# Optimization experiments

Measured on AMD Instinct MI355X. Metric: run time of the kernel, lower is better.

Reference implementation:

```python
import jax, jax.numpy as jnp
import numpy as np

N = 50000        # num_nodes
E = 800000       # num edges (avg degree 16)
IN = 512         # embedding_dim[0]
H = 128          # hidden_dim = embedding_dim[1]
C = 64           # out_dim = n_classes = embedding_dim[-1]
L = 3            # layer_num = len(embedding_dim) - 1


def _lin(k, fan_in, fan_out):
    s = 1.0 / np.sqrt(fan_in)
    k1, k2 = jax.random.split(k)
    W = jax.random.uniform(k1, (fan_in, fan_out), jnp.float32, -s, s)
    b = jax.random.uniform(k2, (fan_out,), jnp.float32, -s, s)
    return W, b


def setup_inputs() -> dict:
    key = jax.random.key(0)
    ks = jax.random.split(key, 12)
    d = {}
    d["x"] = jax.random.normal(ks[0], (N, IN), jnp.float32)
    d["edge_index"] = jax.random.randint(ks[1], (2, E), 0, N)
    # pseudo_mlp: in_dim -> 512 -> 64 -> out_dim
    d["Wp1"], d["bp1"] = _lin(ks[2], IN, 512)
    d["Wp2"], d["bp2"] = _lin(ks[3], 512, 64)
    d["Wp3"], d["bp3"] = _lin(ks[4], 64, C)
    # parsing_mats[0] (only ln=0 is used in learn_soft_edge3), init ones/scaling_factor
    d["parsing0"] = jnp.ones((C, C), jnp.float32) / 2.0 + 0.01 * jax.random.normal(ks[5], (C, C), jnp.float32)
    # GCNConv weights (PyG style: linear without bias, bias added after aggregation)
    d["Wg0"], d["bg0"] = _lin(ks[6], IN, H)
    d["Wg1"], d["bg1"] = _lin(ks[7], H, H)
    d["Wg2"], d["bg2"] = _lin(ks[8], H, H)
    # JK 'cat' -> lin1 input is (layer_num-1)*hidden
    d["Wl1"], d["bl1"] = _lin(ks[9], (L - 1) * H, H)
    d["Wl2"], d["bl2"] = _lin(ks[10], H, C)
    return d


def gcn_conv(x, W, b, edge_index, ew, n):
    """PyG GCNConv with per-edge weight ew, add_self_loops=True (loop weight 1)."""
    xw = x @ W                                           # [N, F_out]
    row, col = edge_index[0], edge_index[1]
    loop = jnp.arange(n)
    row2 = jnp.concatenate([row, loop])
    col2 = jnp.concatenate([col, loop])
    ew2 = jnp.concatenate([ew, jnp.ones((n,), xw.dtype)])
    deg = jax.ops.segment_sum(ew2, col2, num_segments=n)
    dis = jnp.where(deg > 0, jax.lax.rsqrt(deg), 0.0)    # deg^-1/2, inf -> 0
    norm = dis[row2] * ew2 * dis[col2]                   # [E+N]
    out = jax.ops.segment_sum(norm[:, None] * xw[row2], col2, num_segments=n)
    return out + b


def soft_edge_weight(x, edge_index, Wp1, bp1, Wp2, bp2, Wp3, bp3, parsing0):
    """learn_soft_edge3: bilinear form start^T * relu(2*P) * end per edge.
    Original materializes an [E,C,C] outer product then bmm + diagonal; the
    diagonal-sum equals einsum('ek,ed,dk->e', start, end, parsing), computed
    here as a fused small matmul + elementwise reduce (same math)."""
    h = jax.nn.relu(x @ Wp1 + bp1)
    h = jax.nn.relu(h @ Wp2 + bp2)
    logits = h @ Wp3 + bp3                               # [N, C]
    parsing = jax.nn.relu(2.0 * parsing0)                # scaling_factor = 2
    s = logits[edge_index[0]]                            # [E, C] start
    e = logits[edge_index[1]]                            # [E, C] end
    ew = jnp.sum((e @ parsing) * s, axis=-1)             # [E]
    mean = ew.mean()
    var = jnp.var(ew, ddof=1)                            # torch .var() is unbiased
    return (ew - mean) * jnp.sqrt(1e-4 / var) + 1.0


def reference(x, edge_index, Wp1, bp1, Wp2, bp2, Wp3, bp3, parsing0,
              Wg0, bg0, Wg1, bg1, Wg2, bg2, Wl1, bl1, Wl2, bl2):
    n = x.shape[0]
    ew = soft_edge_weight(x, edge_index, Wp1, bp1, Wp2, bp2, Wp3, bp3, parsing0)
    # layer 0
    x1 = jax.nn.relu(gcn_conv(x, Wg0, bg0, edge_index, ew, n))
    xs = [x1]
    # ln = 1 (not last): conv -> relu -> (dropout off in eval) -> append
    x2 = jax.nn.relu(gcn_conv(x1, Wg1, bg1, edge_index, ew, n))
    xs.append(x2)
    # ln = 2 (last layer): computed in original but loop breaks before append;
    # jump(xs) overwrites x, so the last conv's output never reaches the output.
    xj = jnp.concatenate(xs, axis=-1)                    # JK 'cat' -> [N, (L-1)*H]
    out = jax.nn.relu(xj @ Wl1 + bl1)
    out = out @ Wl2 + bl2                                # [N, C]
    return out
```

## Files before the change

### kernel.cpp

```cpp
#include <hip/hip_runtime.h>
#include <hip/hip_bf16.h>
#include <cmath>
#include <cstring>

#define NNODES 50000
#define NEDGES 800000
#define IND    512
#define HD     128
#define CD     64

typedef __bf16 bf16x8 __attribute__((ext_vector_type(8)));
typedef float  f32x4  __attribute__((ext_vector_type(4)));
typedef const __attribute__((address_space(1))) unsigned int* gu32p;
typedef __attribute__((address_space(3))) unsigned int* lu32p;

static const size_t XJ_B   = 0;
static const size_t HID_B  = 25600000;
static const size_t H1_B   = 51200000;
static const size_t XW_B   = 102400000;
static const size_t H2_B   = 115200000;
static const size_t LG_B   = 121600000;
static const size_t PE_B   = 128000000;
static const size_t WT_B   = 134400000;
static const size_t CSRR_B = 135300000;
static const size_t EWC_B  = 138500000;
static const size_t CSRW_B = 141700000;
static const size_t CNT_B  = 144900000;
static const size_t S_B    = 145100000;
static const size_t ZERO_BYTES = 200016;
static const size_t RP_B   = 145100016;
static const size_t WOFF_B = 145300020;
static const size_t INCL_B = 145500020;
static const size_t BSUM_B = 145700020;
static const size_t ST_B   = 145701044;
static const size_t DIS_B  = 145701052;

static const size_t WP1T_O = 0;
static const size_t WG0T_O = 524288;
static const size_t WP2T_O = 655360;
static const size_t WP3T_O = 720896;
static const size_t W2T_O  = 729088;
static const size_t WG1T_O = 737280;
static const size_t WL1T_O = 770048;
static const size_t WL2T_O = 835584;
static const size_t BG1_O  = 851968;
static const size_t BG3_O  = 854528;

struct WD { const float* s; __hip_bfloat16* d; int K; int N; };
struct WP { WD w[7]; };

__global__ __launch_bounds__(256) void transpose_cast_all(WP p)
{
    WD d = p.w[blockIdx.y];
    int i = blockIdx.x * 256 + threadIdx.x;
    if (i >= d.K * d.N) return;
    int k = i % d.K, n = i / d.K;
    d.d[i] = __float2bfloat16(d.s[(size_t)k * d.N + n]);
}

__global__ __launch_bounds__(256) void combine_p0(
    const float* __restrict__ Wp3, const float* __restrict__ bp3,
    const float* __restrict__ P0, const float* __restrict__ bp1,
    __hip_bfloat16* __restrict__ W2t, float* __restrict__ bias_g1,
    float* __restrict__ bias_g3)
{
    int b = blockIdx.x;
    if (b < 16) {
        int i = b * 256 + threadIdx.x;
        int k = i >> 6, n = i & 63;
        float s = 0.f;
        for (int j = 0; j < 64; j++)
            s += Wp3[k * 64 + j] * fmaxf(2.f * P0[j * 64 + n], 0.f);
        W2t[n * 64 + k] = __float2bfloat16(s);
    } else if (b == 16) {
        int n = threadIdx.x;
        if (n < 64) {
            float s = 0.f;
            for (int j = 0; j < 64; j++)
                s += bp3[j] * fmaxf(2.f * P0[j * 64 + n], 0.f);
            bias_g3[n] = bp3[n];
            bias_g3[64 + n] = s;
        }
    } else {
        int i = (b - 17) * 256 + threadIdx.x;
        if (i < 512) bias_g1[i] = bp1[i];
        else if (i < 640) bias_g1[i] = 0.f;
    }
}

template<int BN, int WN, int CAST_A>
__global__ __launch_bounds__(256) void gemm_mfma(
    const void* __restrict__ Ap, int lda,
    const __hip_bfloat16* __restrict__ Bt, int ldb,
    const float* __restrict__ bias,
    void* __restrict__ Cout, int ldc,
    void* __restrict__ Cout2, int ldc2, int splitN,
    int M, int K, int do_relu, int out_bf16)
{
    constexpr int BF = WN / 16;
    constexpr int BPASS = BN / 64;
    constexpr int AST = CAST_A ? 40 : 32;
    __shared__ __bf16 As[128 * AST];
    __shared__ __bf16 Bs[BN * 32];

    const int NC = gridDim.x, NR = gridDim.y;
    int g = blockIdx.y * NC + blockIdx.x;
    int per = NC * 8;
    int nfull = (NR >> 3) * per;
    int rowt, colt;
    if (g < nfull) {
        int grp = g / per, rem = g % per;
        rowt = grp * 8 + (rem & 7);
        colt = rem >> 3;
    } else {
        int rem = g - nfull;
        int tail = NR - (NR >> 3) * 8;
        rowt = (NR >> 3) * 8 + rem % tail;
        colt = rem / tail;
    }

    const int t = threadIdx.x;
    const int row0 = rowt * 128;
    const int col0 = colt * BN;

    const int wv   = t >> 6;
    const int lane = t & 63;
    const int quad = lane >> 4;
    const int l16  = lane & 15;
    const int wrow = (wv >> 1) * 64;
    const int wcol = (wv & 1) * WN;

    const int subrow = lane >> 2;
    const int kchunk = (lane & 3) ^ (subrow & 3);
    const int subkg  = kchunk * 8;

    f32x4 acc[4][BF] = {};

    for (int k0 = 0; k0 < K; k0 += 32) {
        if (CAST_A) {
            const float* Af = (const float*)Ap;
            #pragma unroll
            for (int p = 0; p < 4; p++) {
                int idx = t + p * 256;
                int r = idx >> 3, kg = (idx & 7) * 4;
                int m = row0 + r;
                if (m > M - 1) m = M - 1;
                float4 v = *(const float4*)(Af + (size_t)m * lda + k0 + kg);
                __hip_bfloat16 o[4] __attribute__((aligned(8)));
                o[0] = __float2bfloat16(v.x); o[1] = __float2bfloat16(v.y);
                o[2] = __float2bfloat16(v.z); o[3] = __float2bfloat16(v.w);
                *(int2*)&As[r * AST + kg] = *(const int2*)o;
            }
        } else {
            const __hip_bfloat16* Ab = (const __hip_bfloat16*)Ap;
            #pragma unroll
            for (int p = 0; p < 2; p++) {
                int rowA = (p * 4 + wv) * 16 + subrow;
                const __hip_bfloat16* gp = Ab + (size_t)(row0 + rowA) * lda + k0 + subkg;
                __builtin_amdgcn_global_load_lds((gu32p)(const void*)gp,
                    (lu32p)(void*)&As[(p * 4 + wv) * 512], 16, 0, 0);
            }
        }
        #pragma unroll
        for (int p = 0; p < BPASS; p++) {
            int rowB = (p * 4 + wv) * 16 + subrow;
            const __hip_bfloat16* gp = Bt + (size_t)(col0 + rowB) * ldb + k0 + subkg;
            __builtin_amdgcn_global_load_lds((gu32p)(const void*)gp,
                (lu32p)(void*)&Bs[(p * 4 + wv) * 512], 16, 0, 0);
        }
        __syncthreads();

        bf16x8 af[4], bfr[BF];
        #pragma unroll
        for (int i = 0; i < 4; i++) {
            int R = wrow + i * 16 + l16;
            int c = CAST_A ? quad : (quad ^ (R & 3));
            af[i] = *(const bf16x8*)&As[R * AST + c * 8];
        }
        #pragma unroll
        for (int j = 0; j < BF; j++) {
            int R = wcol + j * 16 + l16;
            bfr[j] = *(const bf16x8*)&Bs[R * 32 + (quad ^ (R & 3)) * 8];
        }
        #pragma unroll
        for (int i = 0; i < 4; i++)
            #pragma unroll
            for (int j = 0; j < BF; j++)
                acc[i][j] = __builtin_amdgcn_mfma_f32_16x16x32_bf16(af[i], bfr[j], acc[i][j], 0, 0, 0);
        __syncthreads();
    }

    #pragma unroll
    for (int i = 0; i < 4; i++) {
        #pragma unroll
        for (int j = 0; j < BF; j++) {
            int n = col0 + wcol + j * 16 + l16;
            bool second = (n >= splitN);
            float bv = bias ? bias[n] : 0.f;
            #pragma unroll
            for (int reg = 0; reg < 4; reg++) {
                int m = row0 + wrow + i * 16 + quad * 4 + reg;
                if (m >= M) continue;
                float v = acc[i][j][reg] + bv;
                if (do_relu && !second) v = fmaxf(v, 0.f);
                if (second)
                    ((__hip_bfloat16*)Cout2)[(size_t)m * ldc2 + (n - splitN)] = __float2bfloat16(v);
                else if (out_bf16)
                    ((__hip_bfloat16*)Cout)[(size_t)m * ldc + n] = __float2bfloat16(v);
                else
                    ((float*)Cout)[(size_t)m * ldc + n] = v;
            }
        }
    }
}

__global__ __launch_bounds__(256) void count_kernel(
    const int* __restrict__ ei, int* __restrict__ cnt)
{
    int e = blockIdx.x * 256 + threadIdx.x;
    if (e >= NEDGES) return;
    atomicAdd(&cnt[ei[NEDGES + e]], 1);
}

__global__ __launch_bounds__(256) void scan1_kernel(
    const int* __restrict__ cnt, int* __restrict__ incl, int* __restrict__ bsum)
{
    __shared__ int s[256];
    int t = threadIdx.x;
    int i = blockIdx.x * 256 + t;
    int v = (i < NNODES) ? cnt[i] : 0;
    s[t] = v;
    __syncthreads();
    for (int off = 1; off < 256; off <<= 1) {
        int u = (t >= off) ? s[t - off] : 0;
        __syncthreads();
        s[t] += u;
        __syncthreads();
    }
    if (i < NNODES) incl[i] = s[t];
    if (t == 255) bsum[blockIdx.x] = s[255];
}

__global__ __launch_bounds__(256) void scan2_kernel(int* __restrict__ bsum, int nb)
{
    __shared__ int s[256];
    int t = threadIdx.x;
    int v = (t < nb) ? bsum[t] : 0;
    s[t] = v;
    __syncthreads();
    for (int off = 1; off < 256; off <<= 1) {
        int u = (t >= off) ? s[t - off] : 0;
        __syncthreads();
        s[t] += u;
        __syncthreads();
    }
    if (t < nb) bsum[t] = s[t] - v;
}

__global__ __launch_bounds__(256) void scan3_kernel(
    const int* __restrict__ cnt, const int* __restrict__ incl,
    const int* __restrict__ bsum, int* __restrict__ rowptr, int* __restrict__ woff)
{
    int i = blockIdx.x * 256 + threadIdx.x;
    if (i >= NNODES) return;
    int off = bsum[blockIdx.x];
    int r = incl[i] - cnt[i] + off;
    rowptr[i] = r;
    woff[i] = r;
    if (i == NNODES - 1) rowptr[NNODES] = incl[i] + off;
}

__global__ __launch_bounds__(256) void scatter_idx_kernel(
    const int* __restrict__ ei, int* __restrict__ woff,
    int* __restrict__ csr_row, int* __restrict__ csr_col)
{
    int e = blockIdx.x * 256 + threadIdx.x;
    if (e >= NEDGES) return;
    int r = ei[e];
    int c = ei[NEDGES + e];
    int p = atomicAdd(&woff[c], 1);
    csr_row[p] = r;
    csr_col[p] = c;
}

__global__ __launch_bounds__(256) void edge_ew_gather(
    const __hip_bfloat16* __restrict__ lg, const __hip_bfloat16* __restrict__ pe,
    const int* __restrict__ csr_row, const int* __restrict__ csr_col,
    float* __restrict__ ew_csr)
{
    const int tid = threadIdx.x;
    const int sub = tid & 7;
    const int e = blockIdx.x * 32 + (tid >> 3);
    if (e >= NEDGES) return;
    int r = csr_row[e];
    int c = csr_col[e];
    bf16x8 a = *(const bf16x8*)(lg + (size_t)r * CD + sub * 8);
    bf16x8 b = *(const bf16x8*)(pe + (size_t)c * CD + sub * 8);
    float acc = 0.f;
    #pragma unroll
    for (int u = 0; u < 8; u++)
        acc += (float)a[u] * (float)b[u];
    acc += __shfl_xor(acc, 1);
    acc += __shfl_xor(acc, 2);
    acc += __shfl_xor(acc, 4);
    if (sub == 0) ew_csr[e] = acc;
}

__global__ __launch_bounds__(256) void ew_stats_kernel(
    const float* __restrict__ ew, double* __restrict__ S)
{
    const int tid = threadIdx.x;
    double s1 = 0.0, s2 = 0.0;
    for (int i = blockIdx.x * 256 + tid; i < NEDGES; i += gridDim.x * 256) {
        float v = ew[i];
        s1 += v; s2 += (double)v * (double)v;
    }
    __shared__ double sh1[256], sh2[256];
    sh1[tid] = s1; sh2[tid] = s2;
    __syncthreads();
    for (int s = 128; s > 0; s >>= 1) {
        if (tid < s) { sh1[tid] += sh1[tid + s]; sh2[tid] += sh2[tid + s]; }
        __syncthreads();
    }
    if (tid == 0) {
        atomicAdd(&S[0], sh1[0]);
        atomicAdd(&S[1], sh2[0]);
    }
}

__global__ void stats_kernel(const double* __restrict__ S, float* __restrict__ st)
{
    double E = (double)NEDGES;
    double mean = S[0] / E;
    double var = (S[1] - S[0] * S[0] / E) / (E - 1.0);
    st[0] = (float)mean;
    st[1] = (float)sqrt(1e-4 / var);
}

__global__ __launch_bounds__(256) void norm_deg_kernel(
    const int* __restrict__ rowptr, float* __restrict__ ew_csr,
    const float* __restrict__ st, float* __restrict__ dis)
{
    int n = blockIdx.x * 256 + threadIdx.x;
    if (n >= NNODES) return;
    float mean = st[0], alpha = st[1];
    int s = rowptr[n], e = rowptr[n + 1];
    float sum = 0.f;
    for (int j = s; j < e; j++) {
        float w = (ew_csr[j] - mean) * alpha + 1.0f;
        ew_csr[j] = w;
        sum += w;
    }
    float d = sum + 1.0f;
    dis[n] = (d > 0.f) ? rsqrtf(d) : 0.f;
}

__global__ __launch_bounds__(256) void csrw_kernel(
    const int* __restrict__ rowptr, const int* __restrict__ csr_row,
    const float* __restrict__ ew_csr, const float* __restrict__ dis,
    float* __restrict__ csr_w)
{
    int n = blockIdx.x * 256 + threadIdx.x;
    if (n >= NNODES) return;
    float dn = dis[n];
    int s = rowptr[n], e = rowptr[n + 1];
    for (int j = s; j < e; j++)
        csr_w[j] = dis[csr_row[j]] * ew_csr[j] * dn;
}

__global__ __launch_bounds__(128) void agg_kernel(
    const unsigned* __restrict__ xw32, const float* __restrict__ dis,
    const int* __restrict__ rowptr, const int* __restrict__ csr_row,
    const float* __restrict__ csr_w, const float* __restrict__ bias,
    __hip_bfloat16* __restrict__ out, int ldo)
{
    const int wv = threadIdx.x >> 6, lane = threadIdx.x & 63;
    const int n = blockIdx.x * 2 + wv;
    if (n >= NNODES) return;
    float dn = dis[n];
    unsigned v0 = xw32[(size_t)n * 64 + lane];
    float aL = dn * dn * __uint_as_float(v0 << 16);
    float aH = dn * dn * __uint_as_float(v0 & 0xffff0000u);
    int s = rowptr[n], e = rowptr[n + 1];
    int j = s;
    for (; j + 4 <= e; j += 4) {
        int r0 = csr_row[j], r1 = csr_row[j + 1];
        int r2 = csr_row[j + 2], r3 = csr_row[j + 3];
        float w0 = csr_w[j], w1 = csr_w[j + 1];
        float w2 = csr_w[j + 2], w3 = csr_w[j + 3];
        unsigned g0 = xw32[(size_t)r0 * 64 + lane];
        unsigned g1 = xw32[(size_t)r1 * 64 + lane];
        unsigned g2 = xw32[(size_t)r2 * 64 + lane];
        unsigned g3 = xw32[(size_t)r3 * 64 + lane];
        aL = fmaf(w0, __uint_as_float(g0 << 16), aL);
        aH = fmaf(w0, __uint_as_float(g0 & 0xffff0000u), aH);
        aL = fmaf(w1, __uint_as_float(g1 << 16), aL);
        aH = fmaf(w1, __uint_as_float(g1 & 0xffff0000u), aH);
        aL = fmaf(w2, __uint_as_float(g2 << 16), aL);
        aH = fmaf(w2, __uint_as_float(g2 & 0xffff0000u), aH);
        aL = fmaf(w3, __uint_as_float(g3 << 16), aL);
        aH = fmaf(w3, __uint_as_float(g3 & 0xffff0000u), aH);
    }
    for (; j < e; j++) {
        int r = csr_row[j];
        float w = csr_w[j];
        unsigned g = xw32[(size_t)r * 64 + lane];
        aL = fmaf(w, __uint_as_float(g << 16), aL);
        aH = fmaf(w, __uint_as_float(g & 0xffff0000u), aH);
    }
    float2 b = *(const float2*)(bias + 2 * lane);
    aL = fmaxf(aL + b.x, 0.f);
    aH = fmaxf(aH + b.y, 0.f);
    __hip_bfloat16 bl = __float2bfloat16(aL), bh = __float2bfloat16(aH);
    unsigned short ul, uh;
    memcpy(&ul, &bl, 2); memcpy(&uh, &bh, 2);
    unsigned o = (unsigned)ul | ((unsigned)uh << 16);
    *(unsigned*)(out + (size_t)n * ldo + 2 * lane) = o;
}

extern "C" void kernel_launch(void* const* d_in, const int* in_sizes, int n_in,
                              void* d_out, int out_size, void* d_ws, size_t ws_size,
                              hipStream_t stream)
{
    const float* x   = (const float*)d_in[0];
    const int*   ei  = (const int*)d_in[1];
    const float* Wp1 = (const float*)d_in[2];
    const float* bp1 = (const float*)d_in[3];
    const float* Wp2 = (const float*)d_in[4];
    const float* bp2 = (const float*)d_in[5];
    const float* Wp3 = (const float*)d_in[6];
    const float* bp3 = (const float*)d_in[7];
    const float* P0  = (const float*)d_in[8];
    const float* Wg0 = (const float*)d_in[9];
    const float* bg0 = (const float*)d_in[10];
    const float* Wg1 = (const float*)d_in[11];
    const float* bg1 = (const float*)d_in[12];
    const float* Wl1 = (const float*)d_in[15];
    const float* bl1 = (const float*)d_in[16];
    const float* Wl2 = (const float*)d_in[17];
    const float* bl2 = (const float*)d_in[18];
    float* out = (float*)d_out;

    char* wsb = (char*)d_ws;
    __hip_bfloat16* xj     = (__hip_bfloat16*)(wsb + XJ_B);
    __hip_bfloat16* hid    = (__hip_bfloat16*)(wsb + HID_B);
    __hip_bfloat16* h1     = (__hip_bfloat16*)(wsb + H1_B);
    __hip_bfloat16* xw     = (__hip_bfloat16*)(wsb + XW_B);
    __hip_bfloat16* h2     = (__hip_bfloat16*)(wsb + H2_B);
    __hip_bfloat16* lg     = (__hip_bfloat16*)(wsb + LG_B);
    __hip_bfloat16* pe     = (__hip_bfloat16*)(wsb + PE_B);
    int*            csr_row= (int*)(wsb + CSRR_B);
    float*          ew_csr = (float*)(wsb + EWC_B);
    int*            csr_col= (int*)(wsb + CSRW_B);
    float*          csr_w  = (float*)(wsb + CSRW_B);
    int*            cnt    = (int*)(wsb + CNT_B);
    double*         S      = (double*)(wsb + S_B);
    int*            rowptr = (int*)(wsb + RP_B);
    int*            woff   = (int*)(wsb + WOFF_B);
    int*            incl   = (int*)(wsb + INCL_B);
    int*            bsum   = (int*)(wsb + BSUM_B);
    float*          st     = (float*)(wsb + ST_B);
    float*          dis    = (float*)(wsb + DIS_B);

    __hip_bfloat16* Wp1t = (__hip_bfloat16*)(wsb + WT_B + WP1T_O);
    __hip_bfloat16* Wg0t = (__hip_bfloat16*)(wsb + WT_B + WG0T_O);
    __hip_bfloat16* Wp2t = (__hip_bfloat16*)(wsb + WT_B + WP2T_O);
    __hip_bfloat16* Wp3t = (__hip_bfloat16*)(wsb + WT_B + WP3T_O);
    __hip_bfloat16* W2t  = (__hip_bfloat16*)(wsb + WT_B + W2T_O);
    __hip_bfloat16* Wg1t = (__hip_bfloat16*)(wsb + WT_B + WG1T_O);
    __hip_bfloat16* Wl1t = (__hip_bfloat16*)(wsb + WT_B + WL1T_O);
    __hip_bfloat16* Wl2t = (__hip_bfloat16*)(wsb + WT_B + WL2T_O);
    float*          bias_g1 = (float*)(wsb + WT_B + BG1_O);
    float*          bias_g3 = (float*)(wsb + WT_B + BG3_O);

    const int EB = (NEDGES + 255) / 256;
    const int NB = (NNODES + 255) / 256;
    const int MT = (NNODES + 127) / 128;
    const int BIGN = 1 << 30;

    hipMemsetAsync(wsb + CNT_B, 0, ZERO_BYTES, stream);

    WP wp;
    wp.w[0] = { Wp1, Wp1t, 512, 512 };
    wp.w[1] = { Wg0, Wg0t, 512, 128 };
    wp.w[2] = { Wp2, Wp2t, 512,  64 };
    wp.w[3] = { Wp3, Wp3t,  64,  64 };
    wp.w[4] = { Wg1, Wg1t, 128, 128 };
    wp.w[5] = { Wl1, Wl1t, 256, 128 };
    wp.w[6] = { Wl2, Wl2t, 128,  64 };
    transpose_cast_all<<<dim3(1024, 7), 256, 0, stream>>>(wp);
    combine_p0<<<20, 256, 0, stream>>>(Wp3, bp3, P0, bp1, W2t, bias_g1, bias_g3);

    count_kernel<<<EB, 256, 0, stream>>>(ei, cnt);
    scan1_kernel<<<NB, 256, 0, stream>>>(cnt, incl, bsum);
    scan2_kernel<<<1, 256, 0, stream>>>(bsum, NB);
    scan3_kernel<<<NB, 256, 0, stream>>>(cnt, incl, bsum, rowptr, woff);
    scatter_idx_kernel<<<EB, 256, 0, stream>>>(ei, woff, csr_row, csr_col);

    gemm_mfma<128, 64, 1><<<dim3(5, MT), 256, 0, stream>>>(
        x, 512, Wp1t, 512, bias_g1, h1, 512, xw, 128, 512, NNODES, 512, 1, 1);

    gemm_mfma<64, 32, 0><<<dim3(1, MT), 256, 0, stream>>>(
        h1, 512, Wp2t, 512, bp2, h2, 64, nullptr, 0, BIGN, NNODES, 512, 1, 1);

    gemm_mfma<128, 64, 0><<<dim3(1, MT), 256, 0, stream>>>(
        h2, 64, Wp3t, 64, bias_g3, lg, 64, pe, 64, 64, NNODES, 64, 0, 1);

    edge_ew_gather<<<(NEDGES + 31) / 32, 256, 0, stream>>>(lg, pe, csr_row, csr_col, ew_csr);
    ew_stats_kernel<<<512, 256, 0, stream>>>(ew_csr, S);
    stats_kernel<<<1, 1, 0, stream>>>(S, st);
    norm_deg_kernel<<<NB, 256, 0, stream>>>(rowptr, ew_csr, st, dis);
    csrw_kernel<<<NB, 256, 0, stream>>>(rowptr, csr_row, ew_csr, dis, csr_w);

    agg_kernel<<<25000, 128, 0, stream>>>((const unsigned*)xw, dis, rowptr, csr_row, csr_w, bg0, xj, 2 * HD);

    gemm_mfma<64, 32, 0><<<dim3(2, MT), 256, 0, stream>>>(
        xj, 2 * HD, Wg1t, 128, nullptr, xw, 128, nullptr, 0, BIGN, NNODES, 128, 0, 1);
    agg_kernel<<<25000, 128, 0, stream>>>((const unsigned*)xw, dis, rowptr, csr_row, csr_w, bg1, xj + HD, 2 * HD);

    gemm_mfma<128, 64, 0><<<dim3(1, MT), 256, 0, stream>>>(
        xj, 2 * HD, Wl1t, 256, bl1, hid, 128, nullptr, 0, BIGN, NNODES, 256, 1, 1);
    gemm_mfma<64, 32, 0><<<dim3(1, MT), 256, 0, stream>>>(
        hid, 128, Wl2t, 128, bl2, out, 64, nullptr, 0, BIGN, NNODES, 128, 0, 0);
}
```

Measured before the change: 572.1 us.

## Double-buffer GEMM LDS tiles, pre-cast x to bf16, merge small prep kernels

The GEMM kernel now keeps two LDS buffers, so the async global-to-LDS loads for the next K tile overlap the MFMA work on the current one. The fp32-to-bf16 cast of x moves out of the first GEMM into a combined prep kernel, which also does the weight transposes and the P0 folding. That lets every GEMM use the direct load-to-LDS path. Launch count drops by folding scan2 into scan3 and stats into norm_deg, at the cost of redundant per-block recomputation. The changes add an extra pass that writes and rereads x in bf16, and double the LDS used per block, which can lower occupancy.

```diff
diff --git a/kernel.cpp b/kernel.cpp
--- a/kernel.cpp
+++ b/kernel.cpp
@@ -47,50 +47,73 @@
 static const size_t BG3_O  = 854528;
 
 struct WD { const float* s; __hip_bfloat16* d; int K; int N; };
-struct WP { WD w[7]; };
-
-__global__ __launch_bounds__(256) void transpose_cast_all(WP p)
-{
-    WD d = p.w[blockIdx.y];
-    int i = blockIdx.x * 256 + threadIdx.x;
-    if (i >= d.K * d.N) return;
-    int k = i % d.K, n = i / d.K;
-    d.d[i] = __float2bfloat16(d.s[(size_t)k * d.N + n]);
-}
-
-__global__ __launch_bounds__(256) void combine_p0(
-    const float* __restrict__ Wp3, const float* __restrict__ bp3,
-    const float* __restrict__ P0, const float* __restrict__ bp1,
-    __hip_bfloat16* __restrict__ W2t, float* __restrict__ bias_g1,
-    float* __restrict__ bias_g3)
+struct PrepArgs {
+    const float* x; __hip_bfloat16* xb;
+    WD w[7];
+    int bo[8];
+    const float* Wp3; const float* bp3; const float* P0; const float* bp1;
+    __hip_bfloat16* W2t; float* bias_g1; float* bias_g3;
+};
+#define PREP_CAST_BLKS 12500
+#define PREP_TP_BLKS   1648
+#define PREP_BLKS      (PREP_CAST_BLKS + PREP_TP_BLKS + 20)
+
+__global__ __launch_bounds__(256) void prep_all(PrepArgs a)
 {
     int b = blockIdx.x;
+    int t = threadIdx.x;
+    if (b < PREP_CAST_BLKS) {
+        int i = b * 256 + t;
+        const float4* p = (const float4*)a.x + (size_t)i * 2;
+        float4 u = p[0], v = p[1];
+        __hip_bfloat16 o[8] __attribute__((aligned(16)));
+        o[0] = __float2bfloat16(u.x); o[1] = __float2bfloat16(u.y);
+        o[2] = __float2bfloat16(u.z); o[3] = __float2bfloat16(u.w);
+        o[4] = __float2bfloat16(v.x); o[5] = __float2bfloat16(v.y);
+        o[6] = __float2bfloat16(v.z); o[7] = __float2bfloat16(v.w);
+        *(int4*)(a.xb + (size_t)i * 8) = *(const int4*)o;
+        return;
+    }
+    b -= PREP_CAST_BLKS;
+    if (b < PREP_TP_BLKS) {
+        int m = 0;
+        #pragma unroll
+        for (int q = 1; q < 7; q++) if (b >= a.bo[q]) m = q;
+        WD d = a.w[m];
+        int i = (b - a.bo[m]) * 256 + t;
+        if (i < d.K * d.N) {
+            int k = i % d.K, n = i / d.K;
+            d.d[i] = __float2bfloat16(d.s[(size_t)k * d.N + n]);
+        }
+        return;
+    }
+    b -= PREP_TP_BLKS;
     if (b < 16) {
-        int i = b * 256 + threadIdx.x;
+        int i = b * 256 + t;
         int k = i >> 6, n = i & 63;
         float s = 0.f;
         for (int j = 0; j < 64; j++)
-            s += Wp3[k * 64 + j] * fmaxf(2.f * P0[j * 64 + n], 0.f);
-        W2t[n * 64 + k] = __float2bfloat16(s);
+            s += a.Wp3[k * 64 + j] * fmaxf(2.f * a.P0[j * 64 + n], 0.f);
+        a.W2t[n * 64 + k] = __float2bfloat16(s);
     } else if (b == 16) {
-        int n = threadIdx.x;
+        int n = t;
         if (n < 64) {
             float s = 0.f;
             for (int j = 0; j < 64; j++)
-                s += bp3[j] * fmaxf(2.f * P0[j * 64 + n], 0.f);
-            bias_g3[n] = bp3[n];
-            bias_g3[64 + n] = s;
+                s += a.bp3[j] * fmaxf(2.f * a.P0[j * 64 + n], 0.f);
+            a.bias_g3[n] = a.bp3[n];
+            a.bias_g3[64 + n] = s;
         }
     } else {
-        int i = (b - 17) * 256 + threadIdx.x;
-        if (i < 512) bias_g1[i] = bp1[i];
-        else if (i < 640) bias_g1[i] = 0.f;
-    }
-}
-
-template<int BN, int WN, int CAST_A>
+        int i = (b - 17) * 256 + t;
+        if (i < 512) a.bias_g1[i] = a.bp1[i];
+        else if (i < 640) a.bias_g1[i] = 0.f;
+    }
+}
+
+template<int BN, int WN>
 __global__ __launch_bounds__(256) void gemm_mfma(
-    const void* __restrict__ Ap, int lda,
+    const __hip_bfloat16* __restrict__ Ab, int lda,
     const __hip_bfloat16* __restrict__ Bt, int ldb,
     const float* __restrict__ bias,
     void* __restrict__ Cout, int ldc,
@@ -99,9 +122,8 @@
 {
     constexpr int BF = WN / 16;
     constexpr int BPASS = BN / 64;
-    constexpr int AST = CAST_A ? 40 : 32;
-    __shared__ __bf16 As[128 * AST];
-    __shared__ __bf16 Bs[BN * 32];
+    __shared__ __bf16 As[2][128 * 32];
+    __shared__ __bf16 Bs[2][BN * 32];
 
     const int NC = gridDim.x, NR = gridDim.y;
     int g = blockIdx.y * NC + blockIdx.x;
@@ -136,58 +158,52 @@
 
     f32x4 acc[4][BF] = {};
 
-    for (int k0 = 0; k0 < K; k0 += 32) {
-        if (CAST_A) {
-            const float* Af = (const float*)Ap;
-            #pragma unroll
-            for (int p = 0; p < 4; p++) {
-                int idx = t + p * 256;
-                int r = idx >> 3, kg = (idx & 7) * 4;
-                int m = row0 + r;
-                if (m > M - 1) m = M - 1;
-                float4 v = *(const float4*)(Af + (size_t)m * lda + k0 + kg);
-                __hip_bfloat16 o[4] __attribute__((aligned(8)));
-                o[0] = __float2bfloat16(v.x); o[1] = __float2bfloat16(v.y);
-                o[2] = __float2bfloat16(v.z); o[3] = __float2bfloat16(v.w);
-                *(int2*)&As[r * AST + kg] = *(const int2*)o;
-            }
-        } else {
-            const __hip_bfloat16* Ab = (const __hip_bfloat16*)Ap;
-            #pragma unroll
-            for (int p = 0; p < 2; p++) {
-                int rowA = (p * 4 + wv) * 16 + subrow;
-                const __hip_bfloat16* gp = Ab + (size_t)(row0 + rowA) * lda + k0 + subkg;
-                __builtin_amdgcn_global_load_lds((gu32p)(const void*)gp,
-                    (lu32p)(void*)&As[(p * 4 + wv) * 512], 16, 0, 0);
-            }
+    auto stage = [&](int buf, int k0) {
+        #pragma unroll
+        for (int p = 0; p < 2; p++) {
+            int rowA = (p * 4 + wv) * 16 + subrow;
+            const __hip_bfloat16* gp = Ab + (size_t)(row0 + rowA) * lda + k0 + subkg;
+            __builtin_amdgcn_global_load_lds((gu32p)(const void*)gp,
+                (lu32p)(void*)&As[buf][(p * 4 + wv) * 512], 16, 0, 0);
         }
         #pragma unroll
         for (int p = 0; p < BPASS; p++) {
             int rowB = (p * 4 + wv) * 16 + subrow;
             const __hip_bfloat16* gp = Bt + (size_t)(col0 + rowB) * ldb + k0 + subkg;
             __builtin_amdgcn_global_load_lds((gu32p)(const void*)gp,
-                (lu32p)(void*)&Bs[(p * 4 + wv) * 512], 16, 0, 0);
-        }
-        __syncthreads();
-
+                (lu32p)(void*)&Bs[buf][(p * 4 + wv) * 512], 16, 0, 0);
+        }
+    };
+
+    auto compute = [&](int buf) {
         bf16x8 af[4], bfr[BF];
         #pragma unroll
         for (int i = 0; i < 4; i++) {
             int R = wrow + i * 16 + l16;
-            int c = CAST_A ? quad : (quad ^ (R & 3));
-            af[i] = *(const bf16x8*)&As[R * AST + c * 8];
+            af[i] = *(const bf16x8*)&As[buf][R * 32 + ((quad ^ (R & 3)) * 8)];
         }
         #pragma unroll
         for (int j = 0; j < BF; j++) {
             int R = wcol + j * 16 + l16;
-            bfr[j] = *(const bf16x8*)&Bs[R * 32 + (quad ^ (R & 3)) * 8];
+            bfr[j] = *(const bf16x8*)&Bs[buf][R * 32 + ((quad ^ (R & 3)) * 8)];
         }
         #pragma unroll
         for (int i = 0; i < 4; i++)
             #pragma unroll
             for (int j = 0; j < BF; j++)
                 acc[i][j] = __builtin_amdgcn_mfma_f32_16x16x32_bf16(af[i], bfr[j], acc[i][j], 0, 0, 0);
-        __syncthreads();
+    };
+
+    const int NT = K >> 5;
+    stage(0, 0);
+    __syncthreads();
+    for (int tt = 0; tt < NT; tt += 2) {
+        if (tt + 1 < NT) stage(1, (tt + 1) << 5);
+        compute(0);
+        if (tt + 1 < NT) __syncthreads(); else break;
+        if (tt + 2 < NT) stage(0, (tt + 2) << 5);
+        compute(1);
+        if (tt + 2 < NT) __syncthreads();
     }
 
     #pragma unroll
@@ -241,7 +257,10 @@
     if (t == 255) bsum[blockIdx.x] = s[255];
 }
 
-__global__ __launch_bounds__(256) void scan2_kernel(int* __restrict__ bsum, int nb)
+__global__ __launch_bounds__(256) void scan3_kernel(
+    const int* __restrict__ cnt, const int* __restrict__ incl,
+    const int* __restrict__ bsum, int* __restrict__ rowptr,
+    int* __restrict__ woff, int nb)
 {
     __shared__ int s[256];
     int t = threadIdx.x;
@@ -254,16 +273,9 @@
         s[t] += u;
         __syncthreads();
     }
-    if (t < nb) bsum[t] = s[t] - v;
-}
-
-__global__ __launch_bounds__(256) void scan3_kernel(
-    const int* __restrict__ cnt, const int* __restrict__ incl,
-    const int* __restrict__ bsum, int* __restrict__ rowptr, int* __restrict__ woff)
-{
-    int i = blockIdx.x * 256 + threadIdx.x;
+    int off = s[blockIdx.x] - bsum[blockIdx.x];
+    int i = blockIdx.x * 256 + t;
     if (i >= NNODES) return;
-    int off = bsum[blockIdx.x];
     int r = incl[i] - cnt[i] + off;
     rowptr[i] = r;
     woff[i] = r;
@@ -328,22 +340,17 @@
     }
 }
 
-__global__ void stats_kernel(const double* __restrict__ S, float* __restrict__ st)
-{
-    double E = (double)NEDGES;
-    double mean = S[0] / E;
-    double var = (S[1] - S[0] * S[0] / E) / (E - 1.0);
-    st[0] = (float)mean;
-    st[1] = (float)sqrt(1e-4 / var);
-}
-
 __global__ __launch_bounds__(256) void norm_deg_kernel(
     const int* __restrict__ rowptr, float* __restrict__ ew_csr,
-    const float* __restrict__ st, float* __restrict__ dis)
+    const double* __restrict__ S, float* __restrict__ dis)
 {
     int n = blockIdx.x * 256 + threadIdx.x;
     if (n >= NNODES) return;
-    float mean = st[0], alpha = st[1];
+    const double Ed = (double)NEDGES;
+    double meand = S[0] / Ed;
+    double var = (S[1] - S[0] * S[0] / Ed) / (Ed - 1.0);
+    float mean = (float)meand;
+    float alpha = (float)sqrt(1e-4 / var);
     int s = rowptr[n], e = rowptr[n + 1];
     float sum = 0.f;
     for (int j = s; j < e; j++) {
@@ -443,6 +450,7 @@
 
     char* wsb = (char*)d_ws;
     __hip_bfloat16* xj     = (__hip_bfloat16*)(wsb + XJ_B);
+    __hip_bfloat16* xb16   = (__hip_bfloat16*)(wsb + XJ_B);
     __hip_bfloat16* hid    = (__hip_bfloat16*)(wsb + HID_B);
     __hip_bfloat16* h1     = (__hip_bfloat16*)(wsb + H1_B);
     __hip_bfloat16* xw     = (__hip_bfloat16*)(wsb + XW_B);
@@ -459,7 +467,6 @@
     int*            woff   = (int*)(wsb + WOFF_B);
     int*            incl   = (int*)(wsb + INCL_B);
     int*            bsum   = (int*)(wsb + BSUM_B);
-    float*          st     = (float*)(wsb + ST_B);
     float*          dis    = (float*)(wsb + DIS_B);
 
     __hip_bfloat16* Wp1t = (__hip_bfloat16*)(wsb + WT_B + WP1T_O);
@@ -480,46 +487,48 @@
 
     hipMemsetAsync(wsb + CNT_B, 0, ZERO_BYTES, stream);
 
-    WP wp;
-    wp.w[0] = { Wp1, Wp1t, 512, 512 };
-    wp.w[1] = { Wg0, Wg0t, 512, 128 };
-    wp.w[2] = { Wp2, Wp2t, 512,  64 };
-    wp.w[3] = { Wp3, Wp3t,  64,  64 };
-    wp.w[4] = { Wg1, Wg1t, 128, 128 };
-    wp.w[5] = { Wl1, Wl1t, 256, 128 };
-    wp.w[6] = { Wl2, Wl2t, 128,  64 };
-    transpose_cast_all<<<dim3(1024, 7), 256, 0, stream>>>(wp);
-    combine_p0<<<20, 256, 0, stream>>>(Wp3, bp3, P0, bp1, W2t, bias_g1, bias_g3);
+    PrepArgs pa;
+    pa.x = x; pa.xb = xb16;
+    pa.w[0] = { Wp1, Wp1t, 512, 512 };
+    pa.w[1] = { Wg0, Wg0t, 512, 128 };
+    pa.w[2] = { Wp2, Wp2t, 512,  64 };
+    pa.w[3] = { Wp3, Wp3t,  64,  64 };
+    pa.w[4] = { Wg1, Wg1t, 128, 128 };
+    pa.w[5] = { Wl1, Wl1t, 256, 128 };
+    pa.w[6] = { Wl2, Wl2t, 128,  64 };
+    pa.bo[0] = 0;    pa.bo[1] = 1024; pa.bo[2] = 1280; pa.bo[3] = 1408;
+    pa.bo[4] = 1424; pa.bo[5] = 1488; pa.bo[6] = 1616; pa.bo[7] = 1648;
+    pa.Wp3 = Wp3; pa.bp3 = bp3; pa.P0 = P0; pa.bp1 = bp1;
+    pa.W2t = W2t; pa.bias_g1 = bias_g1; pa.bias_g3 = bias_g3;
+    prep_all<<<PREP_BLKS, 256, 0, stream>>>(pa);
 
     count_kernel<<<EB, 256, 0, stream>>>(ei, cnt);
     scan1_kernel<<<NB, 256, 0, stream>>>(cnt, incl, bsum);
-    scan2_kernel<<<1, 256, 0, stream>>>(bsum, NB);
-    scan3_kernel<<<NB, 256, 0, stream>>>(cnt, incl, bsum, rowptr, woff);
+    scan3_kernel<<<NB, 256, 0, stream>>>(cnt, incl, bsum, rowptr, woff, NB);
     scatter_idx_kernel<<<EB, 256, 0, stream>>>(ei, woff, csr_row, csr_col);
 
-    gemm_mfma<128, 64, 1><<<dim3(5, MT), 256, 0, stream>>>(
-        x, 512, Wp1t, 512, bias_g1, h1, 512, xw, 128, 512, NNODES, 512, 1, 1);
-
-    gemm_mfma<64, 32, 0><<<dim3(1, MT), 256, 0, stream>>>(
+    gemm_mfma<128, 64><<<dim3(5, MT), 256, 0, stream>>>(
+        xb16, 512, Wp1t, 512, bias_g1, h1, 512, xw, 128, 512, NNODES, 512, 1, 1);
+
+    gemm_mfma<64, 32><<<dim3(1, MT), 256, 0, stream>>>(
         h1, 512, Wp2t, 512, bp2, h2, 64, nullptr, 0, BIGN, NNODES, 512, 1, 1);
 
-    gemm_mfma<128, 64, 0><<<dim3(1, MT), 256, 0, stream>>>(
+    gemm_mfma<128, 64><<<dim3(1, MT), 256, 0, stream>>>(
         h2, 64, Wp3t, 64, bias_g3, lg, 64, pe, 64, 64, NNODES, 64, 0, 1);
 
     edge_ew_gather<<<(NEDGES + 31) / 32, 256, 0, stream>>>(lg, pe, csr_row, csr_col, ew_csr);
     ew_stats_kernel<<<512, 256, 0, stream>>>(ew_csr, S);
-    stats_kernel<<<1, 1, 0, stream>>>(S, st);
-    norm_deg_kernel<<<NB, 256, 0, stream>>>(rowptr, ew_csr, st, dis);
+    norm_deg_kernel<<<NB, 256, 0, stream>>>(rowptr, ew_csr, S, dis);
     csrw_kernel<<<NB, 256, 0, stream>>>(rowptr, csr_row, ew_csr, dis, csr_w);
 
     agg_kernel<<<25000, 128, 0, stream>>>((const unsigned*)xw, dis, rowptr, csr_row, csr_w, bg0, xj, 2 * HD);
 
-    gemm_mfma<64, 32, 0><<<dim3(2, MT), 256, 0, stream>>>(
+    gemm_mfma<64, 32><<<dim3(2, MT), 256, 0, stream>>>(
         xj, 2 * HD, Wg1t, 128, nullptr, xw, 128, nullptr, 0, BIGN, NNODES, 128, 0, 1);
     agg_kernel<<<25000, 128, 0, stream>>>((const unsigned*)xw, dis, rowptr, csr_row, csr_w, bg1, xj + HD, 2 * HD);
 
-    gemm_mfma<128, 64, 0><<<dim3(1, MT), 256, 0, stream>>>(
+    gemm_mfma<128, 64><<<dim3(1, MT), 256, 0, stream>>>(
         xj, 2 * HD, Wl1t, 256, bl1, hid, 128, nullptr, 0, BIGN, NNODES, 256, 1, 1);
-    gemm_mfma<64, 32, 0><<<dim3(1, MT), 256, 0, stream>>>(
+    gemm_mfma<64, 32><<<dim3(1, MT), 256, 0, stream>>>(
         hid, 128, Wl2t, 128, bl2, out, 64, nullptr, 0, BIGN, NNODES, 128, 0, 0);
 }
```

Result: slower. 591.4 us (+3.4%).
